# Kernel optimization log

Measured on AMD Instinct MI355X. Metric: run time of the kernel, lower is better.

The kernel has to match this reference:

```python
import jax, jax.numpy as jnp
import numpy as np

D_MODEL = 1024
N_EXPERTS = 8
TOP_K = 2
CAP_FACTOR = 1.0
HIDDEN = 2816  # multiple_of*ceil(int(2*4*d/3)/multiple_of) with multiple_of=256


def setup_inputs() -> dict:
    key = jax.random.key(0)
    ks = jax.random.split(key, 8)
    B, S = 2, 2048
    s = 0.02
    return {
        "x": jax.random.normal(ks[0], (B, S, D_MODEL), jnp.float32),
        "noise": jax.random.normal(ks[1], (B, S, N_EXPERTS), jnp.float32),
        "router_w": jax.random.normal(ks[2], (N_EXPERTS, D_MODEL), jnp.float32) * s,
        "router_b": jnp.zeros((N_EXPERTS,), jnp.float32),
        "noise_w": jax.random.normal(ks[3], (N_EXPERTS, D_MODEL), jnp.float32) * s,
        "noise_b": jnp.zeros((N_EXPERTS,), jnp.float32),
        "w1": jax.random.normal(ks[4], (N_EXPERTS, HIDDEN, D_MODEL), jnp.float32) * s,
        "w3": jax.random.normal(ks[5], (N_EXPERTS, HIDDEN, D_MODEL), jnp.float32) * s,
        "w2": jax.random.normal(ks[6], (N_EXPERTS, D_MODEL, HIDDEN), jnp.float32) * s,
    }


def reference(x, noise, router_w, router_b, noise_w, noise_b, w1, w3, w2):
    B, S, d = x.shape
    N = B * S
    capacity = int(N * TOP_K / N_EXPERTS * CAP_FACTOR)
    flat_x = x.reshape(N, d)

    # noisy top-k router
    logits = flat_x @ router_w.T + router_b                      # [N, E]
    noise_logits = flat_x @ noise_w.T + noise_b                  # [N, E]
    noisy = logits + noise.reshape(N, N_EXPERTS) * jax.nn.softplus(noise_logits)
    topv, topi = jax.lax.top_k(noisy, TOP_K)                     # [N, k]
    # softmax over sparse (-inf filled) logits == softmax over top-k values
    gw = jax.nn.softmax(topv, axis=-1)                           # [N, k]

    updates = jnp.zeros_like(flat_x)
    tok_ids = jnp.arange(N, dtype=jnp.int32)
    for e in range(N_EXPERTS):
        hit = topi == e                                          # [N, k]
        gate = jnp.sum(gw * hit, axis=-1)                        # [N]
        m = jnp.any(hit, axis=-1)                                # token routed to e
        pos = jnp.cumsum(m.astype(jnp.int32)) - 1                # rank in flat order
        keep = m & (pos < capacity)                              # capacity truncation (first-come)
        slot = jnp.where(keep, pos, capacity)                    # dropped tokens -> overflow slot
        # gather tokens into fixed-capacity buffer (slot `capacity` is a trash slot)
        buf = jnp.zeros((capacity + 1, d), x.dtype).at[slot].set(flat_x)
        tok = jnp.full((capacity + 1,), N, jnp.int32).at[slot].set(tok_ids)
        xb = buf[:capacity]
        # SwiGLU FFN: w2( silu(x w1^T) * (x w3^T) )
        h = jax.nn.silu(xb @ w1[e].T) * (xb @ w3[e].T)           # [cap, H]
        o = h @ w2[e].T                                          # [cap, d]
        tke = tok[:capacity]
        g = jnp.where(tke < N, gate[jnp.clip(tke, 0, N - 1)], 0.0)
        # scatter-combine; index N drops (empty slots)
        updates = updates.at[tke].add(o * g[:, None], mode="drop")
    return updates.reshape(B, S, d)
```

## Files before the change

### kernel.cpp

```cpp
#include <hip/hip_runtime.h>


#define D_MODEL 1024
#define HIDDEN 2816
#define N_TOK 4096
#define CAP 1024

typedef __attribute__((ext_vector_type(8))) short short8;
typedef __attribute__((ext_vector_type(4))) float f32x4;

__device__ __forceinline__ unsigned short f2bf(float f) {
  unsigned int u = __float_as_uint(f);
  u += 0x7fffu + ((u >> 16) & 1u);
  return (unsigned short)(u >> 16);
}
__device__ __forceinline__ float bf2f(unsigned short h) {
  return __uint_as_float(((unsigned int)h) << 16);
}

template <int Ncnt> __device__ __forceinline__ void waitv() {
  if constexpr (Ncnt == 8)      asm volatile("s_waitcnt vmcnt(8)" ::: "memory");
  else if constexpr (Ncnt == 6) asm volatile("s_waitcnt vmcnt(6)" ::: "memory");
  else                          asm volatile("s_waitcnt vmcnt(0)" ::: "memory");
}

__global__ void router_kernel(const float* __restrict__ x, const float* __restrict__ noise,
                              const float* __restrict__ rw, const float* __restrict__ rb,
                              const float* __restrict__ nw, const float* __restrict__ nb,
                              int* __restrict__ topi, float* __restrict__ gall,
                              int* __restrict__ slot) {
  int wid = threadIdx.x >> 6;
  int lane = threadIdx.x & 63;
  int t = blockIdx.x * 4 + wid;
  if (t >= N_TOK) return;
  const float* xr = x + (size_t)t * D_MODEL;
  double accL[8] = {0,0,0,0,0,0,0,0};
  double accN[8] = {0,0,0,0,0,0,0,0};
  for (int i = 0; i < 4; ++i) {
    int kb = (i * 64 + lane) * 4;
    float4 xv = *(const float4*)(xr + kb);
#pragma unroll
    for (int e = 0; e < 8; ++e) {
      float4 wv = *(const float4*)(rw + e * D_MODEL + kb);
      accL[e] += (double)xv.x * wv.x + (double)xv.y * wv.y + (double)xv.z * wv.z + (double)xv.w * wv.w;
      float4 nv = *(const float4*)(nw + e * D_MODEL + kb);
      accN[e] += (double)xv.x * nv.x + (double)xv.y * nv.y + (double)xv.z * nv.z + (double)xv.w * nv.w;
    }
  }
#pragma unroll
  for (int e = 0; e < 8; ++e) {
    for (int s = 32; s > 0; s >>= 1) {
      accL[e] += __shfl_xor(accL[e], s);
      accN[e] += __shfl_xor(accN[e], s);
    }
  }
  if (lane == 0) {
    double noisy[8];
#pragma unroll
    for (int e = 0; e < 8; ++e) {
      double lg = accL[e] + (double)rb[e];
      double nl = accN[e] + (double)nb[e];
      double sp = (nl > 0.0 ? nl : 0.0) + log1p(exp(-fabs(nl)));
      noisy[e] = lg + (double)noise[t * 8 + e] * sp;
    }
    int i0 = 0;
    for (int e = 1; e < 8; ++e) if (noisy[e] > noisy[i0]) i0 = e;
    int i1 = -1;
    for (int e = 0; e < 8; ++e) { if (e == i0) continue; if (i1 < 0 || noisy[e] > noisy[i1]) i1 = e; }
    double g0 = 1.0 / (1.0 + exp(noisy[i1] - noisy[i0]));
    topi[t * 2] = i0; topi[t * 2 + 1] = i1;
    gall[t * 2] = (float)g0; gall[t * 2 + 1] = (float)(1.0 - g0);
    slot[t * 2] = -1; slot[t * 2 + 1] = -1;
  }
}

__global__ void scan_kernel(const int* __restrict__ topi, const float* __restrict__ gall,
                            int* __restrict__ slot, int* __restrict__ tok_list,
                            float* __restrict__ gslot) {
  int e = blockIdx.x;
  int tid = threadIdx.x;
  int lane = tid & 63, wid = tid >> 6;
  __shared__ int wsum[16];
  __shared__ int base_s;
  tok_list[e * CAP + tid] = -1;
  if (tid == 0) base_s = 0;
  __syncthreads();
  for (int chunk = 0; chunk < N_TOK / 1024; ++chunk) {
    int t = chunk * 1024 + tid;
    int i0 = topi[t * 2], i1 = topi[t * 2 + 1];
    bool m = (i0 == e) || (i1 == e);
    unsigned long long mask = __ballot(m);
    int excl = __popcll(mask & ((1ull << lane) - 1ull));
    if (lane == 0) wsum[wid] = __popcll(mask);
    __syncthreads();
    int base = base_s;
    int woff = 0;
    for (int w = 0; w < wid; ++w) woff += wsum[w];
    int pos = base + woff + excl;
    if (m && pos < CAP) {
      tok_list[e * CAP + pos] = t;
      gslot[e * CAP + pos] = gall[t * 2 + (i0 == e ? 0 : 1)];
      if (i0 == e) slot[t * 2] = pos; else slot[t * 2 + 1] = pos;
    }
    __syncthreads();
    if (tid == 0) {
      int s = 0;
      for (int w = 0; w < 16; ++w) s += wsum[w];
      base_s = base + s;
    }
    __syncthreads();
  }
}

__global__ void gather_kernel(const float* __restrict__ x, const int* __restrict__ tok_list,
                              unsigned short* __restrict__ xb) {
  int row = blockIdx.x;
  int tok = tok_list[row];
  unsigned short* dst = xb + (size_t)row * D_MODEL + threadIdx.x * 4;
  if (tok < 0) {
    *(ushort4*)dst = make_ushort4(0, 0, 0, 0);
  } else {
    float4 v = *(const float4*)(x + (size_t)tok * D_MODEL + threadIdx.x * 4);
    *(ushort4*)dst = make_ushort4(f2bf(v.x), f2bf(v.y), f2bf(v.z), f2bf(v.w));
  }
}

__global__ void cvt3_kernel(const float* __restrict__ s0, const float* __restrict__ s1,
                            const float* __restrict__ s2, unsigned short* __restrict__ d0,
                            unsigned short* __restrict__ d1, unsigned short* __restrict__ d2) {
  int i = blockIdx.x * blockDim.x + threadIdx.x;
  const float* src = (blockIdx.y == 0) ? s0 : (blockIdx.y == 1) ? s1 : s2;
  unsigned short* dst = (blockIdx.y == 0) ? d0 : (blockIdx.y == 1) ? d1 : d2;
  float4 v = *(const float4*)(src + (size_t)i * 4);
  *(ushort4*)(dst + (size_t)i * 4) = make_ushort4(f2bf(v.x), f2bf(v.y), f2bf(v.z), f2bf(v.w));
}

template <int NOUT, int K, int NW, int MODE>
__global__ __launch_bounds__(512, 1)
void gemm_moe(const unsigned short* __restrict__ Ab, const unsigned short* __restrict__ B0,
              const unsigned short* __restrict__ B1, void* __restrict__ OUT,
              const int* __restrict__ tokl, const float* __restrict__ gslot) {
  constexpr int ABYTES = 32768;
  constexpr int BUFSZ = ABYTES + NW * 16384;
  constexpr int KT = K / 64;
  constexpr int NBN = NOUT / 128;
  constexpr int NWG = 8 * 4 * NBN;
  constexpr int CPW = (32 + NW * 16) / 8;

  __shared__ char smem[2 * BUFSZ];

  int lid = blockIdx.x;
  int swz = (lid & 7) * (NWG / 8) + (lid >> 3);
  int e = swz / (4 * NBN);
  int rem = swz - e * (4 * NBN);
  int bm = rem / NBN;
  int bn = rem - bm * NBN;

  const unsigned short* A = Ab + (size_t)e * CAP * K;
  int tid = threadIdx.x, lane = tid & 63, wid = tid >> 6;
  int wr = wid >> 2, wc = wid & 3;
  int lane15 = lane & 15, lhi = lane >> 4, l7 = lane & 7;

  int lrow = lane >> 3;
  int lcol = ((lane & 7) ^ lrow) * 8;
  const unsigned short* Abase = A + (size_t)(bm * 256 + lrow) * K + lcol;
  const unsigned short* Bb0 = B0 + (size_t)e * NOUT * K + (size_t)(bn * 128 + lrow) * K + lcol;
  const unsigned short* Bb1 = (NW == 2)
      ? B1 + (size_t)e * NOUT * K + (size_t)(bn * 128 + lrow) * K + lcol : Bb0;

  auto STAGE = [&](int ktile, int buf) {
    char* lb = smem + buf * BUFSZ;
#pragma unroll
    for (int i = 0; i < CPW; ++i) {
      int c = wid * CPW + i;
      if (c < 32) {
        const unsigned short* g = Abase + (size_t)(c * 8) * K + ktile * 64;
        __builtin_amdgcn_global_load_lds((const __attribute__((address_space(1))) void*)g,
                                         (__attribute__((address_space(3))) void*)(lb + c * 1024), 16, 0, 0);
      } else {
        int cb2 = c - 32;
        const unsigned short* base = (cb2 >> 4) ? Bb1 : Bb0;
        const unsigned short* g = base + (size_t)((cb2 & 15) * 8) * K + ktile * 64;
        __builtin_amdgcn_global_load_lds((const __attribute__((address_space(1))) void*)g,
                                         (__attribute__((address_space(3))) void*)(lb + ABYTES + cb2 * 1024), 16, 0, 0);
      }
    }
  };

  int sw0 = ((0 + lhi) ^ l7) * 16;
  int sw1 = ((4 + lhi) ^ l7) * 16;

  f32x4 acc[8][NW][2] = {};

  STAGE(0, 0);
  STAGE(1, 1);
  waitv<CPW>();
  __builtin_amdgcn_sched_barrier(0);
  __builtin_amdgcn_s_barrier();
  __builtin_amdgcn_sched_barrier(0);

  for (int kt = 0; kt < KT; ++kt) {
    char* cb = smem + (kt & 1) * BUFSZ;
    short8 a0[8], b0[NW][2], a1[8], b1[NW][2];
#pragma unroll
    for (int w = 0; w < NW; ++w)
#pragma unroll
      for (int n = 0; n < 2; ++n)
        b0[w][n] = *(const short8*)(cb + ABYTES + w * 16384 + wc * 4096 + n * 2048 + lane15 * 128 + sw0);
#pragma unroll
    for (int m = 0; m < 8; ++m)
      a0[m] = *(const short8*)(cb + wr * 16384 + m * 2048 + lane15 * 128 + sw0);
    __builtin_amdgcn_s_setprio(1);
#pragma unroll
    for (int m = 0; m < 8; ++m)
#pragma unroll
      for (int w = 0; w < NW; ++w)
#pragma unroll
        for (int n = 0; n < 2; ++n)
          acc[m][w][n] = __builtin_amdgcn_mfma_f32_16x16x32_bf16(a0[m], b0[w][n], acc[m][w][n], 0, 0, 0);
    __builtin_amdgcn_s_setprio(0);
#pragma unroll
    for (int w = 0; w < NW; ++w)
#pragma unroll
      for (int n = 0; n < 2; ++n)
        b1[w][n] = *(const short8*)(cb + ABYTES + w * 16384 + wc * 4096 + n * 2048 + lane15 * 128 + sw1);
#pragma unroll
    for (int m = 0; m < 8; ++m)
      a1[m] = *(const short8*)(cb + wr * 16384 + m * 2048 + lane15 * 128 + sw1);
    __builtin_amdgcn_sched_barrier(0);
    __builtin_amdgcn_s_barrier();
    __builtin_amdgcn_sched_barrier(0);
    if (kt + 2 < KT) STAGE(kt + 2, kt & 1);
    __builtin_amdgcn_s_setprio(1);
#pragma unroll
    for (int m = 0; m < 8; ++m)
#pragma unroll
      for (int w = 0; w < NW; ++w)
#pragma unroll
        for (int n = 0; n < 2; ++n)
          acc[m][w][n] = __builtin_amdgcn_mfma_f32_16x16x32_bf16(a1[m], b1[w][n], acc[m][w][n], 0, 0, 0);
    __builtin_amdgcn_s_setprio(0);
    if (kt + 2 < KT) waitv<CPW>();
    else if (kt + 1 < KT) waitv<0>();
    __builtin_amdgcn_sched_barrier(0);
    if (kt + 1 < KT) __builtin_amdgcn_s_barrier();
    __builtin_amdgcn_sched_barrier(0);
  }

  if constexpr (MODE == 1) {
    unsigned short* H = (unsigned short*)OUT + (size_t)e * CAP * NOUT;
#pragma unroll
    for (int m = 0; m < 8; ++m) {
#pragma unroll
      for (int n = 0; n < 2; ++n) {
        int row0 = bm * 256 + wr * 128 + m * 16 + lhi * 4;
        int col = bn * 128 + wc * 32 + n * 16 + lane15;
#pragma unroll
        for (int j = 0; j < 4; ++j) {
          float g1 = acc[m][0][n][j];
          float g3 = acc[m][1][n][j];
          float hv = g1 / (1.0f + __expf(-g1)) * g3;
          H[(size_t)(row0 + j) * NOUT + col] = f2bf(hv);
        }
      }
    }
  } else {
    float* out = (float*)OUT;
#pragma unroll
    for (int m = 0; m < 8; ++m) {
#pragma unroll
      for (int n = 0; n < 2; ++n) {
        int row0 = bm * 256 + wr * 128 + m * 16 + lhi * 4;
        int col = bn * 128 + wc * 32 + n * 16 + lane15;
#pragma unroll
        for (int j = 0; j < 4; ++j) {
          int gr = e * CAP + row0 + j;
          int t = tokl[gr];
          if (t >= 0) {
            float g = gslot[gr];
            atomicAdd(out + (size_t)t * D_MODEL + col, g * acc[m][0][n][j]);
          }
        }
      }
    }
  }
}

extern "C" void kernel_launch(void* const* d_in, const int* in_sizes, int n_in,
                              void* d_out, int out_size, void* d_ws, size_t ws_size,
                              hipStream_t stream) {
  const float* x     = (const float*)d_in[0];
  const float* noise = (const float*)d_in[1];
  const float* rw    = (const float*)d_in[2];
  const float* rb    = (const float*)d_in[3];
  const float* nw    = (const float*)d_in[4];
  const float* nb    = (const float*)d_in[5];
  const float* w1    = (const float*)d_in[6];
  const float* w3    = (const float*)d_in[7];
  const float* w2    = (const float*)d_in[8];
  float* out = (float*)d_out;

  char* ws = (char*)d_ws;
  size_t off = 0;
  auto alloc = [&](size_t bytes) -> void* {
    void* p = ws + off;
    off += (bytes + 255) & ~(size_t)255;
    return p;
  };
  const size_t WELEM = (size_t)8 * HIDDEN * D_MODEL;
  unsigned short* wb1 = (unsigned short*)alloc(WELEM * 2);
  unsigned short* wb3 = (unsigned short*)alloc(WELEM * 2);
  unsigned short* wb2 = (unsigned short*)alloc(WELEM * 2);
  unsigned short* xb  = (unsigned short*)alloc((size_t)8 * CAP * D_MODEL * 2);
  unsigned short* h   = (unsigned short*)alloc((size_t)8 * CAP * HIDDEN * 2);
  int*   topi  = (int*)alloc(N_TOK * 2 * 4);
  float* gall  = (float*)alloc(N_TOK * 2 * 4);
  int*   slot  = (int*)alloc(N_TOK * 2 * 4);
  int*   tokl  = (int*)alloc(8 * CAP * 4);
  float* gslot = (float*)alloc(8 * CAP * 4);
  (void)ws_size; (void)in_sizes; (void)n_in; (void)out_size;

  const int n4w = (int)(WELEM / 4);
  cvt3_kernel<<<dim3(n4w / 256, 3), 256, 0, stream>>>(w1, w3, w2, wb1, wb3, wb2);

  router_kernel<<<N_TOK / 4, 256, 0, stream>>>(x, noise, rw, rb, nw, nb, topi, gall, slot);
  scan_kernel<<<8, 1024, 0, stream>>>(topi, gall, slot, tokl, gslot);
  gather_kernel<<<8 * CAP, 256, 0, stream>>>(x, tokl, xb);

  hipMemsetAsync(d_out, 0, (size_t)N_TOK * D_MODEL * 4, stream);

  gemm_moe<HIDDEN, D_MODEL, 2, 1><<<dim3(704), 512, 0, stream>>>(
      xb, wb1, wb3, (void*)h, nullptr, nullptr);

  gemm_moe<D_MODEL, HIDDEN, 1, 2><<<dim3(256), 512, 0, stream>>>(
      h, wb2, nullptr, (void*)out, tokl, gslot);
}
```

Before: 332.6 us.

## Use split-K with 256-wide N tiles in the down-projection GEMM

```diff
diff --git a/kernel.cpp b/kernel.cpp
--- a/kernel.cpp
+++ b/kernel.cpp
@@ -143,18 +143,25 @@
   constexpr int ABYTES = 32768;
   constexpr int BUFSZ = ABYTES + NW * 16384;
   constexpr int KT = K / 64;
-  constexpr int NBN = NOUT / 128;
-  constexpr int NWG = 8 * 4 * NBN;
+  constexpr int SK = (MODE == 2) ? 2 : 1;
+  constexpr int KTS = KT / SK;
+  constexpr int BNCOL = (MODE == 2 && NW == 2) ? 256 : 128;
+  constexpr int NBN = NOUT / BNCOL;
+  constexpr int NWG = 8 * 4 * NBN * SK;
   constexpr int CPW = (32 + NW * 16) / 8;
 
   __shared__ char smem[2 * BUFSZ];
 
   int lid = blockIdx.x;
   int swz = (lid & 7) * (NWG / 8) + (lid >> 3);
-  int e = swz / (4 * NBN);
-  int rem = swz - e * (4 * NBN);
-  int bm = rem / NBN;
-  int bn = rem - bm * NBN;
+  constexpr int PERE = 4 * NBN * SK;
+  int e = swz / PERE;
+  int r = swz - e * PERE;
+  int bm = r / (NBN * SK);
+  int r2 = r - bm * (NBN * SK);
+  int bn = r2 / SK;
+  int sk = r2 - bn * SK;
+  int kt0 = sk * KTS;
 
   const unsigned short* A = Ab + (size_t)e * CAP * K;
   int tid = threadIdx.x, lane = tid & 63, wid = tid >> 6;
@@ -164,9 +171,9 @@
   int lrow = lane >> 3;
   int lcol = ((lane & 7) ^ lrow) * 8;
   const unsigned short* Abase = A + (size_t)(bm * 256 + lrow) * K + lcol;
-  const unsigned short* Bb0 = B0 + (size_t)e * NOUT * K + (size_t)(bn * 128 + lrow) * K + lcol;
+  const unsigned short* Bb0 = B0 + (size_t)e * NOUT * K + (size_t)(bn * BNCOL + lrow) * K + lcol;
   const unsigned short* Bb1 = (NW == 2)
-      ? B1 + (size_t)e * NOUT * K + (size_t)(bn * 128 + lrow) * K + lcol : Bb0;
+      ? B1 + (size_t)e * NOUT * K + (size_t)(bn * BNCOL + lrow) * K + lcol : Bb0;
 
   auto STAGE = [&](int ktile, int buf) {
     char* lb = smem + buf * BUFSZ;
@@ -192,15 +199,15 @@
 
   f32x4 acc[8][NW][2] = {};
 
-  STAGE(0, 0);
-  STAGE(1, 1);
+  STAGE(kt0, 0);
+  STAGE(kt0 + 1, 1);
   waitv<CPW>();
   __builtin_amdgcn_sched_barrier(0);
   __builtin_amdgcn_s_barrier();
   __builtin_amdgcn_sched_barrier(0);
 
-  for (int kt = 0; kt < KT; ++kt) {
-    char* cb = smem + (kt & 1) * BUFSZ;
+  for (int ktl = 0; ktl < KTS; ++ktl) {
+    char* cb = smem + (ktl & 1) * BUFSZ;
     short8 a0[8], b0[NW][2], a1[8], b1[NW][2];
 #pragma unroll
     for (int w = 0; w < NW; ++w)
@@ -230,7 +237,7 @@
     __builtin_amdgcn_sched_barrier(0);
     __builtin_amdgcn_s_barrier();
     __builtin_amdgcn_sched_barrier(0);
-    if (kt + 2 < KT) STAGE(kt + 2, kt & 1);
+    if (ktl + 2 < KTS) STAGE(kt0 + ktl + 2, ktl & 1);
     __builtin_amdgcn_s_setprio(1);
 #pragma unroll
     for (int m = 0; m < 8; ++m)
@@ -240,10 +247,10 @@
         for (int n = 0; n < 2; ++n)
           acc[m][w][n] = __builtin_amdgcn_mfma_f32_16x16x32_bf16(a1[m], b1[w][n], acc[m][w][n], 0, 0, 0);
     __builtin_amdgcn_s_setprio(0);
-    if (kt + 2 < KT) waitv<CPW>();
-    else if (kt + 1 < KT) waitv<0>();
+    if (ktl + 2 < KTS) waitv<CPW>();
+    else if (ktl + 1 < KTS) waitv<0>();
     __builtin_amdgcn_sched_barrier(0);
-    if (kt + 1 < KT) __builtin_amdgcn_s_barrier();
+    if (ktl + 1 < KTS) __builtin_amdgcn_s_barrier();
     __builtin_amdgcn_sched_barrier(0);
   }
 
@@ -269,16 +276,19 @@
 #pragma unroll
     for (int m = 0; m < 8; ++m) {
 #pragma unroll
-      for (int n = 0; n < 2; ++n) {
-        int row0 = bm * 256 + wr * 128 + m * 16 + lhi * 4;
-        int col = bn * 128 + wc * 32 + n * 16 + lane15;
-#pragma unroll
-        for (int j = 0; j < 4; ++j) {
-          int gr = e * CAP + row0 + j;
-          int t = tokl[gr];
-          if (t >= 0) {
-            float g = gslot[gr];
-            atomicAdd(out + (size_t)t * D_MODEL + col, g * acc[m][0][n][j]);
+      for (int w = 0; w < NW; ++w) {
+#pragma unroll
+        for (int n = 0; n < 2; ++n) {
+          int row0 = bm * 256 + wr * 128 + m * 16 + lhi * 4;
+          int col = bn * BNCOL + w * 128 + wc * 32 + n * 16 + lane15;
+#pragma unroll
+          for (int j = 0; j < 4; ++j) {
+            int gr = e * CAP + row0 + j;
+            int t = tokl[gr];
+            if (t >= 0) {
+              float g = gslot[gr];
+              atomicAdd(out + (size_t)t * D_MODEL + col, g * acc[m][w][n][j]);
+            }
           }
         }
       }
@@ -332,6 +342,6 @@
   gemm_moe<HIDDEN, D_MODEL, 2, 1><<<dim3(704), 512, 0, stream>>>(
       xb, wb1, wb3, (void*)h, nullptr, nullptr);
 
-  gemm_moe<D_MODEL, HIDDEN, 1, 2><<<dim3(256), 512, 0, stream>>>(
-      h, wb2, nullptr, (void*)out, tokl, gslot);
-}
+  gemm_moe<D_MODEL, HIDDEN, 2, 2><<<dim3(256), 512, 0, stream>>>(
+      h, wb2, wb2 + (size_t)128 * HIDDEN, (void*)out, tokl, gslot);
+}
```

After: 367.9 us. +10.6%, slower.
